# Optimization experiments

Measured on AMD Instinct MI355X. Metric: run time of the kernel, lower is better.

## Reference

```python
import jax, jax.numpy as jnp
import numpy as np

B, S, D = 32, 256, 128
K = 16          # num_sample (negatives + the positive appended last)
V = 50000       # vocab / num_classes


def setup_inputs() -> dict:
    key = jax.random.key(0)
    k1, k2, k3, k4 = jax.random.split(key, 4)
    return {
        "input_latent": jax.random.normal(k1, (B, S, D), dtype=jnp.float32),
        "target_labels": jax.random.randint(k2, (B, S), 0, V, dtype=jnp.int64),
        "batch_samples": jax.random.randint(k3, (B, S * (K - 1)), 0, V, dtype=jnp.int64),
        "embed_weight": jax.random.normal(k4, (V, D), dtype=jnp.float32),
    }


def reference(input_latent, target_labels, batch_samples, embed_weight):
    b, s, d = input_latent.shape
    out_emb = embed_weight[target_labels]                      # [B,S,D] positives
    neg_emb = embed_weight[batch_samples].reshape(b, s, K - 1, d)
    # Candidates per target position j: K-1 negatives + the positive itself (last)
    samples = jnp.concatenate([neg_emb, out_emb[:, :, None, :]], axis=2)  # [B,S,K,D]
    # sample_rep[b,i,j,k] = latent[b,i] . samples[b,j,k]
    sample_scores = jnp.einsum('bid,bjkd->bijk', input_latent, samples)   # [B,S,S,K]
    # output_rep[b,i,j] = latent[b,i] . out_emb[b,j] (== sample_scores[...,K-1])
    out_scores = jnp.einsum('bid,bjd->bij', input_latent, out_emb)        # [B,S,S]
    # log( exp(out - max) / sum_k exp(sample - max) ) = out - logsumexp(sample)
    lse = jax.scipy.special.logsumexp(sample_scores, axis=3)              # [B,S,S]
    return out_scores - lse
```

## Files before the change

### kernel.cpp

```cpp
#include <hip/hip_runtime.h>
#include <hip/hip_bf16.h>
#include <math.h>

#define BB 32
#define SS 256
#define DD 128
#define KK 16
#define VV 50000
#define SK (SS*KK)

typedef __attribute__((ext_vector_type(8))) short bf16x8;
typedef __attribute__((ext_vector_type(4))) float f32x4;
typedef __attribute__((ext_vector_type(16))) float f32x16;
typedef unsigned short ushort_t;

static __device__ __forceinline__ short f2bf(float f) {
    unsigned u = __float_as_uint(f);
    unsigned r = (u + 0x7fffu + ((u >> 16) & 1u)) >> 16;
    return (short)r;
}

static __device__ __forceinline__ int lds_off(int row, int d) {
    return row * 256 + ((d * 2) ^ ((row & 15) << 4));
}

static __device__ __forceinline__ void gload_lds16(const void* g, void* lds) {
    __builtin_amdgcn_global_load_lds(
        (const __attribute__((address_space(1))) unsigned int*)g,
        (__attribute__((address_space(3))) unsigned int*)lds, 16, 0, 0);
}

#define NEMB (VV*DD)
#define NLAT (BB*SS*DD)
#define NCHUNK ((NEMB+NLAT)/8)

__global__ __launch_bounds__(256)
void convert_kernel(const float* __restrict__ embed,
                    const float* __restrict__ latent,
                    ushort_t* __restrict__ ws_emb,
                    ushort_t* __restrict__ ws_lat)
{
    int i = blockIdx.x * 256 + threadIdx.x;
    if (i >= NCHUNK) return;
    const float* src;
    ushort_t* dst;
    if (i < NEMB / 8) {
        src = embed + (size_t)i * 8;
        dst = ws_emb + (size_t)i * 8;
    } else {
        int k = i - NEMB / 8;
        src = latent + (size_t)k * 8;
        dst = ws_lat + (size_t)k * 8;
    }
    float f[8];
    *(float4*)(f + 0) = ((const float4*)src)[0];
    *(float4*)(f + 4) = ((const float4*)src)[1];
    short o[8];
    #pragma unroll
    for (int e = 0; e < 8; ++e) o[e] = f2bf(f[e]);
    *(bf16x8*)dst = *(bf16x8*)o;
}

#define MT 64
#define NT 128

__global__ __launch_bounds__(256, 3)
void neg_loss_main(const ushort_t* __restrict__ lat_bf,
                   const int*      __restrict__ labels,
                   const int*      __restrict__ samples,
                   const ushort_t* __restrict__ emb_bf,
                   float* __restrict__ out)
{
    __shared__ char ldsB[NT * 256];
    __shared__ char ldsA[MT * 256];

    const int b    = blockIdx.z;
    const int m0   = blockIdx.y * MT;
    const int n0   = blockIdx.x * NT;
    const int tid  = threadIdx.x;
    const int wave = tid >> 6;
    const int lane = tid & 63;
    const int q    = lane & 15;
    const int sub  = lane >> 4;

    #pragma unroll
    for (int t = 0; t < 8; ++t) {
        const int c0 = wave * 32 + t * 4;
        const int c  = c0 + sub;
        const int gc = n0 + c;
        const int j  = gc >> 4;
        const int k  = gc & 15;
        const int idx = (k < 15)
            ? samples[(size_t)b * (SS * (KK - 1)) + j * (KK - 1) + k]
            : labels[b * SS + j];
        const ushort_t* src = emb_bf + (size_t)idx * DD + ((q ^ (c & 15)) << 3);
        gload_lds16(src, ldsB + c0 * 256);
    }

    #pragma unroll
    for (int t = 0; t < 4; ++t) {
        const int r0 = wave * 16 + t * 4;
        const int r  = r0 + sub;
        const ushort_t* src = lat_bf + ((size_t)(b * SS + m0 + r) * DD)
                                     + ((q ^ (r & 15)) << 3);
        gload_lds16(src, ldsA + r0 * 256);
    }

    __syncthreads();

    const int l31 = lane & 31;
    const int hi  = lane >> 5;
    const int rB  = wave * 32 + l31;

    f32x16 acc0 = {}, acc1 = {};
    #pragma unroll
    for (int ks = 0; ks < 8; ++ks) {
        const int d = ks * 16 + hi * 8;
        bf16x8 av  = *(const bf16x8*)(ldsB + lds_off(rB, d));
        bf16x8 bv0 = *(const bf16x8*)(ldsA + lds_off(l31, d));
        bf16x8 bv1 = *(const bf16x8*)(ldsA + lds_off(32 + l31, d));
        acc0 = __builtin_amdgcn_mfma_f32_32x32x16_bf16(av, bv0, acc0, 0, 0, 0);
        acc1 = __builtin_amdgcn_mfma_f32_32x32x16_bf16(av, bv1, acc1, 0, 0, 0);
    }

    const int jb = (n0 >> 4) + wave * 2;
    #pragma unroll
    for (int f = 0; f < 2; ++f) {
        const f32x16 v = f ? acc1 : acc0;
        float pm0 = fmaxf(fmaxf(fmaxf(v[0], v[1]), fmaxf(v[2], v[3])),
                          fmaxf(fmaxf(v[4], v[5]), fmaxf(v[6], v[7])));
        float pm1 = fmaxf(fmaxf(fmaxf(v[8], v[9]), fmaxf(v[10], v[11])),
                          fmaxf(fmaxf(v[12], v[13]), fmaxf(v[14], v[15])));
        float om0 = fmaxf(pm0, __shfl_xor(pm0, 32));
        float om1 = fmaxf(pm1, __shfl_xor(pm1, 32));
        float ps0 = __expf(v[0] - om0) + __expf(v[1] - om0)
                  + __expf(v[2] - om0) + __expf(v[3] - om0)
                  + __expf(v[4] - om0) + __expf(v[5] - om0)
                  + __expf(v[6] - om0) + __expf(v[7] - om0);
        float ps1 = __expf(v[8]  - om1) + __expf(v[9]  - om1)
                  + __expf(v[10] - om1) + __expf(v[11] - om1)
                  + __expf(v[12] - om1) + __expf(v[13] - om1)
                  + __expf(v[14] - om1) + __expf(v[15] - om1);
        float s0 = ps0 + __shfl_xor(ps0, 32);
        float s1 = ps1 + __shfl_xor(ps1, 32);
        float pos0 = __shfl_xor(v[7], 32);
        float pos1 = v[15];
        const float pos = hi ? pos1 : pos0;
        const float om  = hi ? om1  : om0;
        const float s   = hi ? s1   : s0;
        const int i = m0 + f * 32 + l31;
        out[((size_t)b * SS + i) * SS + (jb + hi)] = pos - om - __logf(s);
    }
}

__global__ __launch_bounds__(256)
void neg_loss_fallback(const float* __restrict__ latent,
                       const int*   __restrict__ labels,
                       const int*   __restrict__ samples,
                       const float* __restrict__ embed,
                       float* __restrict__ out)
{
    __shared__ char ldsA[64 * 256];
    __shared__ char ldsB[64 * 256];

    const int b   = blockIdx.z;
    const int m0  = blockIdx.y * 64;
    const int n0  = blockIdx.x * 64;
    const int tid = threadIdx.x;

    {
        const int r  = tid >> 2;
        const int d0 = (tid & 3) * 32;
        const float* src = latent + ((size_t)b * SS + (m0 + r)) * DD + d0;
        float f[32];
        #pragma unroll
        for (int c = 0; c < 8; ++c)
            *(float4*)(f + 4 * c) = ((const float4*)src)[c];
        #pragma unroll
        for (int c = 0; c < 4; ++c) {
            short tmp[8];
            #pragma unroll
            for (int e = 0; e < 8; ++e) tmp[e] = f2bf(f[c * 8 + e]);
            *(bf16x8*)(ldsA + lds_off(r, d0 + c * 8)) = *(bf16x8*)tmp;
        }
    }
    {
        const int c   = tid >> 2;
        const int d0  = (tid & 3) * 32;
        const int col = n0 + c;
        const int j   = col >> 4;
        const int k   = col & 15;
        const int idx = (k < 15) ? samples[(size_t)b * (SS * (KK - 1)) + j * (KK - 1) + k]
                                 : labels[b * SS + j];
        const float* src = embed + (size_t)idx * DD + d0;
        float f[32];
        #pragma unroll
        for (int cc = 0; cc < 8; ++cc)
            *(float4*)(f + 4 * cc) = ((const float4*)src)[cc];
        #pragma unroll
        for (int cc = 0; cc < 4; ++cc) {
            short tmp[8];
            #pragma unroll
            for (int e = 0; e < 8; ++e) tmp[e] = f2bf(f[cc * 8 + e]);
            *(bf16x8*)(ldsB + lds_off(c, d0 + cc * 8)) = *(bf16x8*)tmp;
        }
    }
    __syncthreads();

    const int wave = tid >> 6;
    const int lane = tid & 63;
    const int wm = wave >> 1, wn = wave & 1;
    const int lr = lane & 15;
    const int lk = (lane >> 4) * 8;
    const int sub = lane >> 4;

    f32x4 acc[2][2] = {};
    #pragma unroll
    for (int ks = 0; ks < 4; ++ks) {
        const int d = ks * 32 + lk;
        bf16x8 a[2], bb2[2];
        #pragma unroll
        for (int mf = 0; mf < 2; ++mf)
            a[mf] = *(const bf16x8*)(ldsA + lds_off(wm * 32 + mf * 16 + lr, d));
        #pragma unroll
        for (int nf = 0; nf < 2; ++nf)
            bb2[nf] = *(const bf16x8*)(ldsB + lds_off(wn * 32 + nf * 16 + lr, d));
        #pragma unroll
        for (int mf = 0; mf < 2; ++mf)
            #pragma unroll
            for (int nf = 0; nf < 2; ++nf)
                acc[mf][nf] = __builtin_amdgcn_mfma_f32_16x16x32_bf16(
                    bb2[nf], a[mf], acc[mf][nf], 0, 0, 0);
    }

    #pragma unroll
    for (int mf = 0; mf < 2; ++mf) {
        #pragma unroll
        for (int nf = 0; nf < 2; ++nf) {
            const f32x4 v = acc[mf][nf];
            float mx = fmaxf(fmaxf(v[0], v[1]), fmaxf(v[2], v[3]));
            mx = fmaxf(mx, __shfl_xor(mx, 16));
            mx = fmaxf(mx, __shfl_xor(mx, 32));
            float e = __expf(v[0] - mx) + __expf(v[1] - mx)
                    + __expf(v[2] - mx) + __expf(v[3] - mx);
            e += __shfl_xor(e, 16);
            e += __shfl_xor(e, 32);
            float pos = __shfl(v[3], (lane & 15) | 48);
            if (sub == 0) {
                const int i  = m0 + wm * 32 + mf * 16 + (lane & 15);
                const int jj = (n0 >> 4) + wn * 2 + nf;
                out[((size_t)b * SS + i) * SS + jj] = pos - mx - __logf(e);
            }
        }
    }
}

extern "C" void kernel_launch(void* const* d_in, const int* in_sizes, int n_in,
                              void* d_out, int out_size, void* d_ws, size_t ws_size,
                              hipStream_t stream) {
    const float* latent  = (const float*)d_in[0];
    const int*   labels  = (const int*)d_in[1];
    const int*   samples = (const int*)d_in[2];
    const float* embed   = (const float*)d_in[3];
    float* out = (float*)d_out;

    const size_t ws_needed = (size_t)(NEMB + NLAT) * 2;
    if (ws_size >= ws_needed) {
        ushort_t* ws_emb = (ushort_t*)d_ws;
        ushort_t* ws_lat = ws_emb + NEMB;
        convert_kernel<<<(NCHUNK + 255) / 256, 256, 0, stream>>>(
            embed, latent, ws_emb, ws_lat);
        dim3 grid(SK / NT, SS / MT, BB);
        neg_loss_main<<<grid, dim3(256), 0, stream>>>(
            ws_lat, labels, samples, ws_emb, out);
    } else {
        dim3 grid(SK / 64, SS / 64, BB);
        neg_loss_fallback<<<grid, dim3(256), 0, stream>>>(
            latent, labels, samples, embed, out);
    }
}
```

Measured before the change: 39.17 us.

## Gather fp32 embeddings directly into registers and loop over M tiles

Drops the full-vocabulary embedding bf16 conversion and converts only the latent tensor. Each thread gathers its candidate embedding row in fp32 straight into registers and converts it to bf16 A-fragments once. Each block then loops over all four M tiles of latent, double-buffering the LDS loads. This avoids converting 50000x128 embeddings every call and reuses the gathered rows across M instead of regathering per tile, at the cost of more registers, fewer blocks, and uncoalesced fp32 row gathers.

```diff
diff --git a/kernel.cpp b/kernel.cpp
--- a/kernel.cpp
+++ b/kernel.cpp
@@ -30,126 +30,140 @@
         (__attribute__((address_space(3))) unsigned int*)lds, 16, 0, 0);
 }
 
-#define NEMB (VV*DD)
 #define NLAT (BB*SS*DD)
-#define NCHUNK ((NEMB+NLAT)/8)
+#define NCHUNK_LAT (NLAT/8)
 
 __global__ __launch_bounds__(256)
-void convert_kernel(const float* __restrict__ embed,
-                    const float* __restrict__ latent,
-                    ushort_t* __restrict__ ws_emb,
-                    ushort_t* __restrict__ ws_lat)
+void convert_lat_kernel(const float* __restrict__ latent,
+                        ushort_t* __restrict__ ws_lat)
 {
     int i = blockIdx.x * 256 + threadIdx.x;
-    if (i >= NCHUNK) return;
-    const float* src;
-    ushort_t* dst;
-    if (i < NEMB / 8) {
-        src = embed + (size_t)i * 8;
-        dst = ws_emb + (size_t)i * 8;
-    } else {
-        int k = i - NEMB / 8;
-        src = latent + (size_t)k * 8;
-        dst = ws_lat + (size_t)k * 8;
-    }
+    if (i >= NCHUNK_LAT) return;
+    const float* src = latent + (size_t)i * 8;
     float f[8];
     *(float4*)(f + 0) = ((const float4*)src)[0];
     *(float4*)(f + 4) = ((const float4*)src)[1];
     short o[8];
     #pragma unroll
     for (int e = 0; e < 8; ++e) o[e] = f2bf(f[e]);
-    *(bf16x8*)dst = *(bf16x8*)o;
+    *(bf16x8*)(ws_lat + (size_t)i * 8) = *(bf16x8*)o;
 }
 
 #define MT 64
 #define NT 128
 
-__global__ __launch_bounds__(256, 3)
+__global__ __launch_bounds__(256)
 void neg_loss_main(const ushort_t* __restrict__ lat_bf,
                    const int*      __restrict__ labels,
                    const int*      __restrict__ samples,
-                   const ushort_t* __restrict__ emb_bf,
+                   const float*    __restrict__ embed,
                    float* __restrict__ out)
 {
-    __shared__ char ldsB[NT * 256];
-    __shared__ char ldsA[MT * 256];
+    __shared__ char ldsA[2][MT * 256];
 
     const int b    = blockIdx.z;
-    const int m0   = blockIdx.y * MT;
     const int n0   = blockIdx.x * NT;
     const int tid  = threadIdx.x;
     const int wave = tid >> 6;
     const int lane = tid & 63;
     const int q    = lane & 15;
     const int sub  = lane >> 4;
-
-    #pragma unroll
-    for (int t = 0; t < 8; ++t) {
-        const int c0 = wave * 32 + t * 4;
-        const int c  = c0 + sub;
-        const int gc = n0 + c;
-        const int j  = gc >> 4;
-        const int k  = gc & 15;
-        const int idx = (k < 15)
-            ? samples[(size_t)b * (SS * (KK - 1)) + j * (KK - 1) + k]
-            : labels[b * SS + j];
-        const ushort_t* src = emb_bf + (size_t)idx * DD + ((q ^ (c & 15)) << 3);
-        gload_lds16(src, ldsB + c0 * 256);
-    }
+    const int l31  = lane & 31;
+    const int hi   = lane >> 5;
+
+    const int rB  = wave * 32 + l31;
+    const int gc  = n0 + rB;
+    const int j   = gc >> 4;
+    const int k   = gc & 15;
+    const int idx = (k < 15)
+        ? samples[(size_t)b * (SS * (KK - 1)) + j * (KK - 1) + k]
+        : labels[b * SS + j];
 
     #pragma unroll
     for (int t = 0; t < 4; ++t) {
         const int r0 = wave * 16 + t * 4;
         const int r  = r0 + sub;
-        const ushort_t* src = lat_bf + ((size_t)(b * SS + m0 + r) * DD)
+        const ushort_t* src = lat_bf + ((size_t)(b * SS + r) * DD)
                                      + ((q ^ (r & 15)) << 3);
-        gload_lds16(src, ldsA + r0 * 256);
+        gload_lds16(src, ldsA[0] + r0 * 256);
+    }
+
+    const float* rowp = embed + (size_t)idx * DD + hi * 8;
+    f32x4 fb[16];
+    #pragma unroll
+    for (int ks = 0; ks < 8; ++ks) {
+        fb[2 * ks]     = *(const f32x4*)(rowp + ks * 16);
+        fb[2 * ks + 1] = *(const f32x4*)(rowp + ks * 16 + 4);
+    }
+    bf16x8 av[8];
+    #pragma unroll
+    for (int ks = 0; ks < 8; ++ks) {
+        short t8[8];
+        #pragma unroll
+        for (int e = 0; e < 4; ++e) t8[e]     = f2bf(fb[2 * ks][e]);
+        #pragma unroll
+        for (int e = 0; e < 4; ++e) t8[4 + e] = f2bf(fb[2 * ks + 1][e]);
+        av[ks] = *(bf16x8*)t8;
     }
 
     __syncthreads();
 
-    const int l31 = lane & 31;
-    const int hi  = lane >> 5;
-    const int rB  = wave * 32 + l31;
-
-    f32x16 acc0 = {}, acc1 = {};
-    #pragma unroll
-    for (int ks = 0; ks < 8; ++ks) {
-        const int d = ks * 16 + hi * 8;
-        bf16x8 av  = *(const bf16x8*)(ldsB + lds_off(rB, d));
-        bf16x8 bv0 = *(const bf16x8*)(ldsA + lds_off(l31, d));
-        bf16x8 bv1 = *(const bf16x8*)(ldsA + lds_off(32 + l31, d));
-        acc0 = __builtin_amdgcn_mfma_f32_32x32x16_bf16(av, bv0, acc0, 0, 0, 0);
-        acc1 = __builtin_amdgcn_mfma_f32_32x32x16_bf16(av, bv1, acc1, 0, 0, 0);
-    }
-
     const int jb = (n0 >> 4) + wave * 2;
-    #pragma unroll
-    for (int f = 0; f < 2; ++f) {
-        const f32x16 v = f ? acc1 : acc0;
-        float pm0 = fmaxf(fmaxf(fmaxf(v[0], v[1]), fmaxf(v[2], v[3])),
-                          fmaxf(fmaxf(v[4], v[5]), fmaxf(v[6], v[7])));
-        float pm1 = fmaxf(fmaxf(fmaxf(v[8], v[9]), fmaxf(v[10], v[11])),
-                          fmaxf(fmaxf(v[12], v[13]), fmaxf(v[14], v[15])));
-        float om0 = fmaxf(pm0, __shfl_xor(pm0, 32));
-        float om1 = fmaxf(pm1, __shfl_xor(pm1, 32));
-        float ps0 = __expf(v[0] - om0) + __expf(v[1] - om0)
-                  + __expf(v[2] - om0) + __expf(v[3] - om0)
-                  + __expf(v[4] - om0) + __expf(v[5] - om0)
-                  + __expf(v[6] - om0) + __expf(v[7] - om0);
-        float ps1 = __expf(v[8]  - om1) + __expf(v[9]  - om1)
-                  + __expf(v[10] - om1) + __expf(v[11] - om1)
-                  + __expf(v[12] - om1) + __expf(v[13] - om1)
-                  + __expf(v[14] - om1) + __expf(v[15] - om1);
-        float s0 = ps0 + __shfl_xor(ps0, 32);
-        float s1 = ps1 + __shfl_xor(ps1, 32);
-        float pos0 = __shfl_xor(v[7], 32);
-        float pos1 = v[15];
-        const float pos = hi ? pos1 : pos0;
-        const float om  = hi ? om1  : om0;
-        const float s   = hi ? s1   : s0;
-        const int i = m0 + f * 32 + l31;
-        out[((size_t)b * SS + i) * SS + (jb + hi)] = pos - om - __logf(s);
+
+    for (int mt = 0; mt < 4; ++mt) {
+        const int cur = mt & 1;
+
+        if (mt < 3) {
+            #pragma unroll
+            for (int t = 0; t < 4; ++t) {
+                const int r0 = wave * 16 + t * 4;
+                const int r  = r0 + sub;
+                const ushort_t* src = lat_bf
+                    + ((size_t)(b * SS + ((mt + 1) * MT + r)) * DD)
+                    + ((q ^ (r & 15)) << 3);
+                gload_lds16(src, ldsA[cur ^ 1] + r0 * 256);
+            }
+        }
+
+        f32x16 acc0 = {}, acc1 = {};
+        #pragma unroll
+        for (int ks = 0; ks < 8; ++ks) {
+            const int d = ks * 16 + hi * 8;
+            bf16x8 bv0 = *(const bf16x8*)(ldsA[cur] + lds_off(l31, d));
+            bf16x8 bv1 = *(const bf16x8*)(ldsA[cur] + lds_off(32 + l31, d));
+            acc0 = __builtin_amdgcn_mfma_f32_32x32x16_bf16(av[ks], bv0, acc0, 0, 0, 0);
+            acc1 = __builtin_amdgcn_mfma_f32_32x32x16_bf16(av[ks], bv1, acc1, 0, 0, 0);
+        }
+
+        #pragma unroll
+        for (int f = 0; f < 2; ++f) {
+            const f32x16 v = f ? acc1 : acc0;
+            float pm0 = fmaxf(fmaxf(fmaxf(v[0], v[1]), fmaxf(v[2], v[3])),
+                              fmaxf(fmaxf(v[4], v[5]), fmaxf(v[6], v[7])));
+            float pm1 = fmaxf(fmaxf(fmaxf(v[8], v[9]), fmaxf(v[10], v[11])),
+                              fmaxf(fmaxf(v[12], v[13]), fmaxf(v[14], v[15])));
+            float om0 = fmaxf(pm0, __shfl_xor(pm0, 32));
+            float om1 = fmaxf(pm1, __shfl_xor(pm1, 32));
+            float ps0 = __expf(v[0] - om0) + __expf(v[1] - om0)
+                      + __expf(v[2] - om0) + __expf(v[3] - om0)
+                      + __expf(v[4] - om0) + __expf(v[5] - om0)
+                      + __expf(v[6] - om0) + __expf(v[7] - om0);
+            float ps1 = __expf(v[8]  - om1) + __expf(v[9]  - om1)
+                      + __expf(v[10] - om1) + __expf(v[11] - om1)
+                      + __expf(v[12] - om1) + __expf(v[13] - om1)
+                      + __expf(v[14] - om1) + __expf(v[15] - om1);
+            float s0 = ps0 + __shfl_xor(ps0, 32);
+            float s1 = ps1 + __shfl_xor(ps1, 32);
+            float pos0 = __shfl_xor(v[7], 32);
+            float pos1 = v[15];
+            const float pos = hi ? pos1 : pos0;
+            const float om  = hi ? om1  : om0;
+            const float s   = hi ? s1   : s0;
+            const int i = mt * MT + f * 32 + l31;
+            out[((size_t)b * SS + i) * SS + (jb + hi)] = pos - om - __logf(s);
+        }
+
+        __syncthreads();
     }
 }
 
@@ -264,15 +278,14 @@
     const float* embed   = (const float*)d_in[3];
     float* out = (float*)d_out;
 
-    const size_t ws_needed = (size_t)(NEMB + NLAT) * 2;
+    const size_t ws_needed = (size_t)NLAT * 2;
     if (ws_size >= ws_needed) {
-        ushort_t* ws_emb = (ushort_t*)d_ws;
-        ushort_t* ws_lat = ws_emb + NEMB;
-        convert_kernel<<<(NCHUNK + 255) / 256, 256, 0, stream>>>(
-            embed, latent, ws_emb, ws_lat);
-        dim3 grid(SK / NT, SS / MT, BB);
+        ushort_t* ws_lat = (ushort_t*)d_ws;
+        convert_lat_kernel<<<(NCHUNK_LAT + 255) / 256, 256, 0, stream>>>(
+            latent, ws_lat);
+        dim3 grid(SK / NT, 1, BB);
         neg_loss_main<<<grid, dim3(256), 0, stream>>>(
-            ws_lat, labels, samples, ws_emb, out);
+            ws_lat, labels, samples, embed, out);
     } else {
         dim3 grid(SK / 64, SS / 64, BB);
         neg_loss_fallback<<<grid, dim3(256), 0, stream>>>(
```

After: 35.62 us. -9.1%, faster.
